# Kernel optimization log

Hardware: AMD Instinct MI355X
Metric: run time of the kernel (lower is better)

## Reference

```python
import jax, jax.numpy as jnp
import numpy as np

P = 256  # patch_size (init kwarg)


def _unfold3s2(g):
    # g: [B,1,P,P] -> [B,9,L], kernel 3, stride 2, torch Unfold ordering (kh outer, kw inner)
    B = g.shape[0]
    n = (P - 3) // 2 + 1
    cols = [g[:, 0, di:di + 2 * n - 1:2, dj:dj + 2 * n - 1:2]
            for di in range(3) for dj in range(3)]  # each [B,n,n]
    return jnp.stack(cols, axis=1).reshape(B, 9, n * n)


def _fold3s2(patches):
    # patches: [..., 9, L] -> [..., P, P], overlap-add (torch Fold, kernel 3, stride 2)
    lead = patches.shape[:-2]
    n = (P - 3) // 2 + 1
    p = patches.reshape(*lead, 3, 3, n, n)
    out = jnp.zeros((*lead, P, P), patches.dtype)
    for di in range(3):
        for dj in range(3):
            out = out.at[..., di:di + 2 * n - 1:2, dj:dj + 2 * n - 1:2].add(p[..., di, dj, :, :])
    return out


def _maxpool3x3(x):
    # MaxPool2d(3, stride=1, padding=1) on NCHW
    return jax.lax.reduce_window(x, -jnp.inf, jax.lax.max,
                                 (1, 1, 3, 3), (1, 1, 1, 1),
                                 [(0, 0), (0, 0), (1, 1), (1, 1)])


def setup_inputs() -> dict:
    key = jax.random.key(0)
    k1, k2 = jax.random.split(key)
    x = jax.random.uniform(k1, (2, 3, P, P), dtype=jnp.float32)
    ref = jax.random.uniform(k2, (2, 3, P, P), dtype=jnp.float32)
    return {"x": x, "ref": ref, "k": 4}


def reference(x, ref, k):
    B = x.shape[0]
    L = ((P - 3) // 2 + 1) ** 2
    # grayscale proxies
    x_gray = jnp.max(_maxpool3x3(x), axis=1, keepdims=True) - jnp.min(x, axis=1, keepdims=True)
    ref_gray = jnp.mean(ref, axis=1, keepdims=True)
    input_patch = _unfold3s2(x_gray)   # [B,9,L]
    ref_patch = _unfold3s2(ref_gray)   # [B,9,L]
    # faithful to original: mean over patch index (dim 2), norm of UNCENTERED patches over dim 1
    input_norm = (input_patch - jnp.mean(input_patch, axis=2, keepdims=True)) \
        / jnp.linalg.norm(input_patch, axis=1, keepdims=True)
    ref_norm = (ref_patch - jnp.mean(ref_patch, axis=2, keepdims=True)) \
        / jnp.linalg.norm(ref_patch, axis=1, keepdims=True)
    ncc = jnp.einsum('bpl,bpm->blm', input_norm, ref_norm)  # [B,L,L]
    _, idx = jax.lax.top_k(ncc, k)                           # idx: [B,L,k]
    # gather best-matching ref patches for all k at once: [B,k,9,L]
    idx_t = jnp.transpose(idx, (0, 2, 1))                    # [B,k,L]
    ind = jnp.broadcast_to(idx_t[:, :, None, :], (B, k, 9, L))
    src = jnp.broadcast_to(ref_patch[:, None], (B, k, 9, L))
    gathered = jnp.take_along_axis(src, ind, axis=3)         # [B,k,9,L]
    folded = _fold3s2(gathered)                              # [B,k,P,P]
    return jnp.concatenate([x, folded], axis=1)              # [B,3+k,P,P]
```

## Files before the change

kernel.cpp:

```cpp
#include <hip/hip_runtime.h>
#include <math.h>
#include <float.h>

#define PSZ 256
#define NPATCH 127
#define L 16129
#define KTOP 4
#define TMAIN 256
#define RPT 2
#define ROWS_PER_BLOCK (TMAIN * RPT)
#define NROWBLK 32
#define NS 32
#define SEGLEN 505
#define MSTRIDE 508
#define ROWPAD 16384
#define GRP 8

typedef float f2 __attribute__((ext_vector_type(2)));

static constexpr size_t OFF_CMAX = 0;
static constexpr size_t OFF_CMIN = OFF_CMAX + 2 * PSZ * PSZ;
static constexpr size_t OFF_REFG = OFF_CMIN + 2 * PSZ * PSZ;
static constexpr size_t OFF_XG   = OFF_REFG + 2 * PSZ * PSZ;
static constexpr size_t OFF_MUI  = OFF_XG   + 2 * PSZ * PSZ;
static constexpr size_t OFF_MUR  = OFF_MUI  + 20;
static constexpr size_t OFF_A    = OFF_MUR  + 20;
static constexpr size_t OFF_B    = OFF_A    + 290324;
static constexpr size_t OFF_BT   = OFF_B    + 290324;
static constexpr size_t OFF_IDX  = OFF_BT   + 290324;
static constexpr size_t OFF_G4   = OFF_IDX  + 2 * L * 4;
static constexpr size_t OFF_PV   = OFF_G4   + 2 * L * 4;
static constexpr size_t OFF_PI   = OFF_PV   + (size_t)2 * NS * ROWPAD * 4;

__device__ __forceinline__ void insg(float rm, int gb,
    float& g0, float& g1, float& g2, float& g3,
    int& i0, int& i1, int& i2, int& i3) {
  bool c0 = rm > g0, c1 = rm > g1, c2 = rm > g2, c3 = rm > g3;
  g3 = c2 ? g2 : (c3 ? rm : g3);  i3 = c2 ? i2 : (c3 ? gb : i3);
  g2 = c1 ? g1 : (c2 ? rm : g2);  i2 = c1 ? i1 : (c2 ? gb : i2);
  g1 = c0 ? g0 : (c1 ? rm : g1);  i1 = c0 ? i0 : (c1 ? gb : i1);
  g0 = c0 ? rm : g0;              i0 = c0 ? gb : i0;
}

__device__ __forceinline__ void ins4c(float v, int m,
    float& v0, float& v1, float& v2, float& v3,
    int& x0, int& x1, int& x2, int& x3) {
  bool c0 = (v > v0) || (v == v0 && m < x0);
  bool c1 = (v > v1) || (v == v1 && m < x1);
  bool c2 = (v > v2) || (v == v2 && m < x2);
  bool c3 = (v > v3) || (v == v3 && m < x3);
  v3 = c2 ? v2 : (c3 ? v : v3);  x3 = c2 ? x2 : (c3 ? m : x3);
  v2 = c1 ? v1 : (c2 ? v : v2);  x2 = c1 ? x1 : (c2 ? m : x2);
  v1 = c0 ? v0 : (c1 ? v : v1);  x1 = c0 ? x0 : (c1 ? m : x1);
  v0 = c0 ? v : v0;              x0 = c0 ? m : x0;
}

__global__ void k1_pixel(const float* __restrict__ x, const float* __restrict__ ref,
                         float* __restrict__ ws, float* __restrict__ out) {
  int id = blockIdx.x * 256 + threadIdx.x;
  if (id >= 2 * PSZ * PSZ) return;
  int b = id >> 16;
  int pix = id & 0xFFFF;
  const float* xb = x + (size_t)b * 3 * PSZ * PSZ + pix;
  float c0 = xb[0], c1 = xb[PSZ * PSZ], c2 = xb[2 * PSZ * PSZ];
  ws[OFF_CMAX + id] = fmaxf(fmaxf(c0, c1), c2);
  ws[OFF_CMIN + id] = fminf(fminf(c0, c1), c2);
  const float* rb = ref + (size_t)b * 3 * PSZ * PSZ + pix;
  ws[OFF_REFG + id] = (rb[0] + rb[PSZ * PSZ] + rb[2 * PSZ * PSZ]) / 3.0f;
  float* ob = out + (size_t)b * 7 * PSZ * PSZ + pix;
  ob[0] = c0; ob[PSZ * PSZ] = c1; ob[2 * PSZ * PSZ] = c2;
}

__global__ void k2_gray(float* __restrict__ ws) {
  int id = blockIdx.x * 256 + threadIdx.x;
  if (id >= 2 * PSZ * PSZ) return;
  int b = id >> 16;
  int pix = id & 0xFFFF;
  int y = pix >> 8, xx = pix & 255;
  const float* cm = ws + OFF_CMAX + ((size_t)b << 16);
  float m = -3.402823466e+38f;
  for (int dy = -1; dy <= 1; ++dy) {
    int yy = y + dy;
    if (yy < 0 || yy > 255) continue;
    for (int dx = -1; dx <= 1; ++dx) {
      int xc = xx + dx;
      if (xc < 0 || xc > 255) continue;
      m = fmaxf(m, cm[yy * PSZ + xc]);
    }
  }
  ws[OFF_XG + id] = m - ws[OFF_CMIN + id];
}

__global__ void k4_mean(float* __restrict__ ws) {
  __shared__ double sm[256];
  int which = blockIdx.x / 18;
  int bp = blockIdx.x % 18;
  int b = bp / 9, p = bp % 9;
  int di = p / 3, dj = p % 3;
  const float* g = ws + (which ? OFF_REFG : OFF_XG) + ((size_t)b << 16);
  double s = 0.0;
  for (int l = threadIdx.x; l < L; l += 256) {
    int i = l / NPATCH, j = l % NPATCH;
    s += (double)g[(2 * i + di) * PSZ + 2 * j + dj];
  }
  sm[threadIdx.x] = s;
  __syncthreads();
  for (int st = 128; st > 0; st >>= 1) {
    if ((int)threadIdx.x < st) sm[threadIdx.x] += sm[threadIdx.x + st];
    __syncthreads();
  }
  if (threadIdx.x == 0)
    ws[(which ? OFF_MUR : OFF_MUI) + bp] = (float)(sm[0] / (double)L);
}

__global__ void k5_norm(float* __restrict__ ws) {
  int id = blockIdx.x * 256 + threadIdx.x;
  if (id >= 2 * L) return;
  int b = id / L, l = id % L;
  int i = l / NPATCH, j = l % NPATCH;
  const float* xg = ws + OFF_XG + ((size_t)b << 16);
  const float* rg = ws + OFF_REFG + ((size_t)b << 16);
  float vi[9], vr[9];
  float si = 0.f, sr = 0.f;
#pragma unroll
  for (int p = 0; p < 9; ++p) {
    int di = p / 3, dj = p % 3;
    vi[p] = xg[(2 * i + di) * PSZ + 2 * j + dj];
    vr[p] = rg[(2 * i + di) * PSZ + 2 * j + dj];
    si += vi[p] * vi[p];
    sr += vr[p] * vr[p];
  }
  float ni = sqrtf(si), nr = sqrtf(sr);
#pragma unroll
  for (int p = 0; p < 9; ++p) {
    float mi = ws[OFF_MUI + b * 9 + p];
    float mr = ws[OFF_MUR + b * 9 + p];
    float bn = (vr[p] - mr) / nr;
    ws[OFF_A + ((size_t)b * L + l) * 9 + p] = (vi[p] - mi) / ni;
    ws[OFF_B + ((size_t)b * 9 + p) * L + l] = bn;
    ws[OFF_BT + ((size_t)b * L + l) * 9 + p] = bn;
  }
}

__global__ __launch_bounds__(TMAIN, 2) void k6_topk(float* __restrict__ ws) {
  __shared__ float lds[9 * MSTRIDE];

  int bid = blockIdx.x;
  int seg = bid % NS;
  int rowblk = (bid / NS) % NROWBLK;
  int b = bid / (NS * NROWBLK);
  int m0 = seg * SEGLEN;
  int mend = m0 + SEGLEN;
  if (mend > L) mend = L;
  int mlen = mend - m0;

  const float* Bg = ws + OFF_B + (size_t)b * 9 * L + m0;
  for (int p = 0; p < 9; ++p)
    for (int mm = threadIdx.x; mm < mlen; mm += TMAIN)
      lds[p * MSTRIDE + mm] = Bg[(size_t)p * L + mm];
  __syncthreads();

  int row0 = rowblk * ROWS_PER_BLOCK + threadIdx.x * RPT;
  int r0 = row0 < L - 1 ? row0 : L - 1;
  int r1 = row0 + 1 < L - 1 ? row0 + 1 : L - 1;
  float a0[9], a1[9];
  {
    const float* Ap0 = ws + OFF_A + ((size_t)b * L + r0) * 9;
    const float* Ap1 = ws + OFF_A + ((size_t)b * L + r1) * 9;
#pragma unroll
    for (int p = 0; p < 9; ++p) { a0[p] = Ap0[p]; a1[p] = Ap1[p]; }
  }

  float g00 = -FLT_MAX, g01 = g00, g02 = g00, g03 = g00;
  float g10 = g00, g11 = g00, g12 = g00, g13 = g00;
  int i00 = 0, i01 = 0, i02 = 0, i03 = 0;
  int i10 = 0, i11 = 0, i12 = 0, i13 = 0;

  int ngrp = mlen >> 3;
  for (int g = 0; g < ngrp; ++g) {
    int mm = g << 3;
    f2 s0a, s0b, s0c, s0d, s1a, s1b, s1c, s1d;
#pragma unroll
    for (int p = 0; p < 9; ++p) {
      const float* base = &lds[p * MSTRIDE + mm];
      f2 b0 = *(const f2*)(base + 0);
      f2 b1 = *(const f2*)(base + 2);
      f2 b2 = *(const f2*)(base + 4);
      f2 b3 = *(const f2*)(base + 6);
      f2 va = {a0[p], a0[p]};
      f2 vb = {a1[p], a1[p]};
      if (p == 0) {
        s0a = va * b0; s0b = va * b1; s0c = va * b2; s0d = va * b3;
        s1a = vb * b0; s1b = vb * b1; s1c = vb * b2; s1d = vb * b3;
      } else {
        s0a = __builtin_elementwise_fma(va, b0, s0a);
        s0b = __builtin_elementwise_fma(va, b1, s0b);
        s0c = __builtin_elementwise_fma(va, b2, s0c);
        s0d = __builtin_elementwise_fma(va, b3, s0d);
        s1a = __builtin_elementwise_fma(vb, b0, s1a);
        s1b = __builtin_elementwise_fma(vb, b1, s1b);
        s1c = __builtin_elementwise_fma(vb, b2, s1c);
        s1d = __builtin_elementwise_fma(vb, b3, s1d);
      }
    }
    f2 rv0 = __builtin_elementwise_max(__builtin_elementwise_max(s0a, s0b),
                                       __builtin_elementwise_max(s0c, s0d));
    f2 rv1 = __builtin_elementwise_max(__builtin_elementwise_max(s1a, s1b),
                                       __builtin_elementwise_max(s1c, s1d));
    float rm0 = fmaxf(rv0.x, rv0.y);
    float rm1 = fmaxf(rv1.x, rv1.y);
    int gb = m0 + mm;
    insg(rm0, gb, g00, g01, g02, g03, i00, i01, i02, i03);
    insg(rm1, gb, g10, g11, g12, g13, i10, i11, i12, i13);
  }
  int tb = ngrp << 3;
  if (tb < mlen) {
    float rt0 = -FLT_MAX, rt1 = -FLT_MAX;
    for (int mm = tb; mm < mlen; ++mm) {
      float bb = lds[mm];
      float sv0 = a0[0] * bb, sv1 = a1[0] * bb;
#pragma unroll
      for (int p = 1; p < 9; ++p) {
        bb = lds[p * MSTRIDE + mm];
        sv0 = fmaf(a0[p], bb, sv0); sv1 = fmaf(a1[p], bb, sv1);
      }
      rt0 = fmaxf(rt0, sv0); rt1 = fmaxf(rt1, sv1);
    }
    insg(rt0, m0 + tb, g00, g01, g02, g03, i00, i01, i02, i03);
    insg(rt1, m0 + tb, g10, g11, g12, g13, i10, i11, i12, i13);
  }

  int* wsi = (int*)ws;
  if (row0 < L) {
    size_t base = (((size_t)b * NS + seg) * ROWPAD + row0) * 4;
    ws[OFF_PV + base + 0] = g00; ws[OFF_PV + base + 1] = g01;
    ws[OFF_PV + base + 2] = g02; ws[OFF_PV + base + 3] = g03;
    wsi[OFF_PI + base + 0] = i00; wsi[OFF_PI + base + 1] = i01;
    wsi[OFF_PI + base + 2] = i02; wsi[OFF_PI + base + 3] = i03;
  }
  if (row0 + 1 < L) {
    size_t base = (((size_t)b * NS + seg) * ROWPAD + row0 + 1) * 4;
    ws[OFF_PV + base + 0] = g10; ws[OFF_PV + base + 1] = g11;
    ws[OFF_PV + base + 2] = g12; ws[OFF_PV + base + 3] = g13;
    wsi[OFF_PI + base + 0] = i10; wsi[OFF_PI + base + 1] = i11;
    wsi[OFF_PI + base + 2] = i12; wsi[OFF_PI + base + 3] = i13;
  }
}

__global__ void k7a_groups(float* __restrict__ ws) {
  int id = blockIdx.x * 256 + threadIdx.x;
  if (id >= 2 * L) return;
  int b = id / L, row = id % L;
  float v0 = -FLT_MAX, v1 = v0, v2 = v0, v3 = v0;
  int x0 = 0x7FFFFFFF, x1 = x0, x2 = x0, x3 = x0;
  const int* wsi_c = (const int*)ws;
  for (int s = 0; s < NS; ++s) {
    size_t base = (((size_t)b * NS + s) * ROWPAD + row) * 4;
#pragma unroll
    for (int q = 0; q < 4; ++q) {
      float val = ws[OFF_PV + base + q];
      int gb = wsi_c[OFF_PI + base + q];
      ins4c(val, gb, v0, v1, v2, v3, x0, x1, x2, x3);
    }
  }
  int* wsi = (int*)ws;
  size_t gb4 = OFF_G4 + (size_t)id * 4;
  wsi[gb4] = x0; wsi[gb4 + 1] = x1; wsi[gb4 + 2] = x2; wsi[gb4 + 3] = x3;
}

__global__ void k7b_recover(float* __restrict__ ws) {
  int id = blockIdx.x * 256 + threadIdx.x;
  if (id >= 2 * L) return;
  int b = id / L, row = id % L;
  float a[9];
  const float* Ap = ws + OFF_A + ((size_t)b * L + row) * 9;
#pragma unroll
  for (int p = 0; p < 9; ++p) a[p] = Ap[p];
  const int* wsi_c = (const int*)ws;
  float v0 = -FLT_MAX, v1 = v0, v2 = v0, v3 = v0;
  int x0 = 0x7FFFFFFF, x1 = x0, x2 = x0, x3 = x0;
#pragma unroll
  for (int slot = 0; slot < 4; ++slot) {
    int gb = wsi_c[OFF_G4 + (size_t)id * 4 + slot];
    int ge = gb + GRP; if (ge > L) ge = L;
    for (int mm = gb; mm < ge; ++mm) {
      const float* bt = ws + OFF_BT + ((size_t)b * L + mm) * 9;
      float s = a[0] * bt[0];
#pragma unroll
      for (int p = 1; p < 9; ++p) s = fmaf(a[p], bt[p], s);
      ins4c(s, mm, v0, v1, v2, v3, x0, x1, x2, x3);
    }
  }
  int* wsi = (int*)ws;
  size_t ib = OFF_IDX + (size_t)id * 4;
  wsi[ib] = x0; wsi[ib + 1] = x1; wsi[ib + 2] = x2; wsi[ib + 3] = x3;
}

__global__ void k8_fold(const float* __restrict__ ws, float* __restrict__ out) {
  int id = blockIdx.x * 256 + threadIdx.x;
  if (id >= 2 * KTOP * PSZ * PSZ) return;
  int b = id / (KTOP * PSZ * PSZ);
  int rem = id % (KTOP * PSZ * PSZ);
  int kk = rem >> 16;
  int pix = rem & 0xFFFF;
  int y = pix >> 8, xx = pix & 255;
  const int* wsi = (const int*)ws;
  const float* rg = ws + OFF_REFG + ((size_t)b << 16);
  float acc = 0.f;
  for (int di = 0; di < 3; ++di) {
    int yy = y - di;
    if (yy < 0 || (yy & 1) || (yy >> 1) >= NPATCH) continue;
    int i = yy >> 1;
    for (int dj = 0; dj < 3; ++dj) {
      int xc = xx - dj;
      if (xc < 0 || (xc & 1) || (xc >> 1) >= NPATCH) continue;
      int j = xc >> 1;
      int l = i * NPATCH + j;
      int m = wsi[OFF_IDX + ((size_t)b * L + l) * 4 + kk];
      int mi = m / NPATCH, mj = m % NPATCH;
      acc += rg[(2 * mi + di) * PSZ + 2 * mj + dj];
    }
  }
  out[(((size_t)b * 7 + 3 + kk) * PSZ + y) * PSZ + xx] = acc;
}

extern "C" void kernel_launch(void* const* d_in, const int* in_sizes, int n_in,
                              void* d_out, int out_size, void* d_ws, size_t ws_size,
                              hipStream_t stream) {
  const float* x = (const float*)d_in[0];
  const float* ref = (const float*)d_in[1];
  float* ws = (float*)d_ws;
  float* out = (float*)d_out;

  k1_pixel<<<512, 256, 0, stream>>>(x, ref, ws, out);
  k2_gray<<<512, 256, 0, stream>>>(ws);
  k4_mean<<<36, 256, 0, stream>>>(ws);
  k5_norm<<<(2 * L + 255) / 256, 256, 0, stream>>>(ws);
  k6_topk<<<2 * NROWBLK * NS, TMAIN, 0, stream>>>(ws);
  k7a_groups<<<(2 * L + 255) / 256, 256, 0, stream>>>(ws);
  k7b_recover<<<(2 * L + 255) / 256, 256, 0, stream>>>(ws);
  k8_fold<<<(2 * KTOP * PSZ * PSZ + 255) / 256, 256, 0, stream>>>(ws, out);
}
```

Baseline: 244.5 us.

## Fuse top-k merge kernels, use packed FMA asm, widen mean reduction

Merges the group-merge and recovery kernels into one, dropping the intermediate group-index buffer and one launch. The top-k inner loop now uses inline v_pk_fma/v_pk_mul asm with float4 LDS loads and pre-splatted A vectors, and replaces the packed max tree with scalar fmaxf. Launch bounds on the top-k kernel are relaxed to one block per SIMD, trading occupancy for registers. The mean kernel uses 1024 threads with contiguous 16-element chunks per thread.

```diff
diff --git a/kernel.cpp b/kernel.cpp
--- a/kernel.cpp
+++ b/kernel.cpp
@@ -18,6 +18,17 @@
 
 typedef float f2 __attribute__((ext_vector_type(2)));
 
+__device__ __forceinline__ f2 pk_fma(f2 a, f2 b, f2 c) {
+  f2 d;
+  asm("v_pk_fma_f32 %0, %1, %2, %3" : "=v"(d) : "v"(a), "v"(b), "v"(c));
+  return d;
+}
+__device__ __forceinline__ f2 pk_mul(f2 a, f2 b) {
+  f2 d;
+  asm("v_pk_mul_f32 %0, %1, %2" : "=v"(d) : "v"(a), "v"(b));
+  return d;
+}
+
 static constexpr size_t OFF_CMAX = 0;
 static constexpr size_t OFF_CMIN = OFF_CMAX + 2 * PSZ * PSZ;
 static constexpr size_t OFF_REFG = OFF_CMIN + 2 * PSZ * PSZ;
@@ -28,8 +39,7 @@
 static constexpr size_t OFF_B    = OFF_A    + 290324;
 static constexpr size_t OFF_BT   = OFF_B    + 290324;
 static constexpr size_t OFF_IDX  = OFF_BT   + 290324;
-static constexpr size_t OFF_G4   = OFF_IDX  + 2 * L * 4;
-static constexpr size_t OFF_PV   = OFF_G4   + 2 * L * 4;
+static constexpr size_t OFF_PV   = OFF_IDX  + 2 * L * 4;
 static constexpr size_t OFF_PI   = OFF_PV   + (size_t)2 * NS * ROWPAD * 4;
 
 __device__ __forceinline__ void insg(float rm, int gb,
@@ -92,24 +102,30 @@
 }
 
 __global__ void k4_mean(float* __restrict__ ws) {
-  __shared__ double sm[256];
+  __shared__ double sm[1024];
   int which = blockIdx.x / 18;
   int bp = blockIdx.x % 18;
   int b = bp / 9, p = bp % 9;
   int di = p / 3, dj = p % 3;
   const float* g = ws + (which ? OFF_REFG : OFF_XG) + ((size_t)b << 16);
+  int t = threadIdx.x;
   double s = 0.0;
-  for (int l = threadIdx.x; l < L; l += 256) {
-    int i = l / NPATCH, j = l % NPATCH;
-    s += (double)g[(2 * i + di) * PSZ + 2 * j + dj];
-  }
-  sm[threadIdx.x] = s;
+  int l0 = t * 16;
+  if (l0 < L) {
+    int l1 = l0 + 16 < L ? l0 + 16 : L;
+    int i = l0 / NPATCH, j = l0 % NPATCH;
+    for (int l = l0; l < l1; ++l) {
+      s += (double)g[(2 * i + di) * PSZ + 2 * j + dj];
+      if (++j == NPATCH) { j = 0; ++i; }
+    }
+  }
+  sm[t] = s;
   __syncthreads();
-  for (int st = 128; st > 0; st >>= 1) {
-    if ((int)threadIdx.x < st) sm[threadIdx.x] += sm[threadIdx.x + st];
+  for (int st = 512; st > 0; st >>= 1) {
+    if (t < st) sm[t] += sm[t + st];
     __syncthreads();
   }
-  if (threadIdx.x == 0)
+  if (t == 0)
     ws[(which ? OFF_MUR : OFF_MUI) + bp] = (float)(sm[0] / (double)L);
 }
 
@@ -142,7 +158,7 @@
   }
 }
 
-__global__ __launch_bounds__(TMAIN, 2) void k6_topk(float* __restrict__ ws) {
+__global__ __launch_bounds__(TMAIN, 1) void k6_topk(float* __restrict__ ws) {
   __shared__ float lds[9 * MSTRIDE];
 
   int bid = blockIdx.x;
@@ -163,12 +179,16 @@
   int row0 = rowblk * ROWS_PER_BLOCK + threadIdx.x * RPT;
   int r0 = row0 < L - 1 ? row0 : L - 1;
   int r1 = row0 + 1 < L - 1 ? row0 + 1 : L - 1;
-  float a0[9], a1[9];
+  f2 va[9], vb[9];
   {
     const float* Ap0 = ws + OFF_A + ((size_t)b * L + r0) * 9;
     const float* Ap1 = ws + OFF_A + ((size_t)b * L + r1) * 9;
 #pragma unroll
-    for (int p = 0; p < 9; ++p) { a0[p] = Ap0[p]; a1[p] = Ap1[p]; }
+    for (int p = 0; p < 9; ++p) {
+      float a0 = Ap0[p], a1 = Ap1[p];
+      va[p].x = a0; va[p].y = a0;
+      vb[p].x = a1; vb[p].y = a1;
+    }
   }
 
   float g00 = -FLT_MAX, g01 = g00, g02 = g00, g03 = g00;
@@ -182,33 +202,26 @@
     f2 s0a, s0b, s0c, s0d, s1a, s1b, s1c, s1d;
 #pragma unroll
     for (int p = 0; p < 9; ++p) {
-      const float* base = &lds[p * MSTRIDE + mm];
-      f2 b0 = *(const f2*)(base + 0);
-      f2 b1 = *(const f2*)(base + 2);
-      f2 b2 = *(const f2*)(base + 4);
-      f2 b3 = *(const f2*)(base + 6);
-      f2 va = {a0[p], a0[p]};
-      f2 vb = {a1[p], a1[p]};
+      const float4* bp4 = reinterpret_cast<const float4*>(&lds[p * MSTRIDE + mm]);
+      float4 q0 = bp4[0], q1 = bp4[1];
+      f2 b0 = {q0.x, q0.y}, b1 = {q0.z, q0.w};
+      f2 b2 = {q1.x, q1.y}, b3 = {q1.z, q1.w};
       if (p == 0) {
-        s0a = va * b0; s0b = va * b1; s0c = va * b2; s0d = va * b3;
-        s1a = vb * b0; s1b = vb * b1; s1c = vb * b2; s1d = vb * b3;
+        s0a = pk_mul(va[0], b0); s0b = pk_mul(va[0], b1);
+        s0c = pk_mul(va[0], b2); s0d = pk_mul(va[0], b3);
+        s1a = pk_mul(vb[0], b0); s1b = pk_mul(vb[0], b1);
+        s1c = pk_mul(vb[0], b2); s1d = pk_mul(vb[0], b3);
       } else {
-        s0a = __builtin_elementwise_fma(va, b0, s0a);
-        s0b = __builtin_elementwise_fma(va, b1, s0b);
-        s0c = __builtin_elementwise_fma(va, b2, s0c);
-        s0d = __builtin_elementwise_fma(va, b3, s0d);
-        s1a = __builtin_elementwise_fma(vb, b0, s1a);
-        s1b = __builtin_elementwise_fma(vb, b1, s1b);
-        s1c = __builtin_elementwise_fma(vb, b2, s1c);
-        s1d = __builtin_elementwise_fma(vb, b3, s1d);
+        s0a = pk_fma(va[p], b0, s0a); s0b = pk_fma(va[p], b1, s0b);
+        s0c = pk_fma(va[p], b2, s0c); s0d = pk_fma(va[p], b3, s0d);
+        s1a = pk_fma(vb[p], b0, s1a); s1b = pk_fma(vb[p], b1, s1b);
+        s1c = pk_fma(vb[p], b2, s1c); s1d = pk_fma(vb[p], b3, s1d);
       }
     }
-    f2 rv0 = __builtin_elementwise_max(__builtin_elementwise_max(s0a, s0b),
-                                       __builtin_elementwise_max(s0c, s0d));
-    f2 rv1 = __builtin_elementwise_max(__builtin_elementwise_max(s1a, s1b),
-                                       __builtin_elementwise_max(s1c, s1d));
-    float rm0 = fmaxf(rv0.x, rv0.y);
-    float rm1 = fmaxf(rv1.x, rv1.y);
+    float rm0 = fmaxf(fmaxf(fmaxf(s0a.x, s0a.y), fmaxf(s0b.x, s0b.y)),
+                      fmaxf(fmaxf(s0c.x, s0c.y), fmaxf(s0d.x, s0d.y)));
+    float rm1 = fmaxf(fmaxf(fmaxf(s1a.x, s1a.y), fmaxf(s1b.x, s1b.y)),
+                      fmaxf(fmaxf(s1c.x, s1c.y), fmaxf(s1d.x, s1d.y)));
     int gb = m0 + mm;
     insg(rm0, gb, g00, g01, g02, g03, i00, i01, i02, i03);
     insg(rm1, gb, g10, g11, g12, g13, i10, i11, i12, i13);
@@ -218,11 +231,11 @@
     float rt0 = -FLT_MAX, rt1 = -FLT_MAX;
     for (int mm = tb; mm < mlen; ++mm) {
       float bb = lds[mm];
-      float sv0 = a0[0] * bb, sv1 = a1[0] * bb;
+      float sv0 = va[0].x * bb, sv1 = vb[0].x * bb;
 #pragma unroll
       for (int p = 1; p < 9; ++p) {
         bb = lds[p * MSTRIDE + mm];
-        sv0 = fmaf(a0[p], bb, sv0); sv1 = fmaf(a1[p], bb, sv1);
+        sv0 = fmaf(va[p].x, bb, sv0); sv1 = fmaf(vb[p].x, bb, sv1);
       }
       rt0 = fmaxf(rt0, sv0); rt1 = fmaxf(rt1, sv1);
     }
@@ -247,13 +260,14 @@
   }
 }
 
-__global__ void k7a_groups(float* __restrict__ ws) {
+__global__ void k7_merge(float* __restrict__ ws) {
   int id = blockIdx.x * 256 + threadIdx.x;
   if (id >= 2 * L) return;
   int b = id / L, row = id % L;
+  const int* wsi_c = (const int*)ws;
+
   float v0 = -FLT_MAX, v1 = v0, v2 = v0, v3 = v0;
   int x0 = 0x7FFFFFFF, x1 = x0, x2 = x0, x3 = x0;
-  const int* wsi_c = (const int*)ws;
   for (int s = 0; s < NS; ++s) {
     size_t base = (((size_t)b * NS + s) * ROWPAD + row) * 4;
 #pragma unroll
@@ -263,37 +277,30 @@
       ins4c(val, gb, v0, v1, v2, v3, x0, x1, x2, x3);
     }
   }
-  int* wsi = (int*)ws;
-  size_t gb4 = OFF_G4 + (size_t)id * 4;
-  wsi[gb4] = x0; wsi[gb4 + 1] = x1; wsi[gb4 + 2] = x2; wsi[gb4 + 3] = x3;
-}
-
-__global__ void k7b_recover(float* __restrict__ ws) {
-  int id = blockIdx.x * 256 + threadIdx.x;
-  if (id >= 2 * L) return;
-  int b = id / L, row = id % L;
+
   float a[9];
   const float* Ap = ws + OFF_A + ((size_t)b * L + row) * 9;
 #pragma unroll
   for (int p = 0; p < 9; ++p) a[p] = Ap[p];
-  const int* wsi_c = (const int*)ws;
-  float v0 = -FLT_MAX, v1 = v0, v2 = v0, v3 = v0;
-  int x0 = 0x7FFFFFFF, x1 = x0, x2 = x0, x3 = x0;
+
+  int gbs[4] = {x0, x1, x2, x3};
+  float w0 = -FLT_MAX, w1 = w0, w2 = w0, w3 = w0;
+  int y0 = 0x7FFFFFFF, y1 = y0, y2 = y0, y3 = y0;
 #pragma unroll
   for (int slot = 0; slot < 4; ++slot) {
-    int gb = wsi_c[OFF_G4 + (size_t)id * 4 + slot];
+    int gb = gbs[slot];
     int ge = gb + GRP; if (ge > L) ge = L;
     for (int mm = gb; mm < ge; ++mm) {
       const float* bt = ws + OFF_BT + ((size_t)b * L + mm) * 9;
       float s = a[0] * bt[0];
 #pragma unroll
       for (int p = 1; p < 9; ++p) s = fmaf(a[p], bt[p], s);
-      ins4c(s, mm, v0, v1, v2, v3, x0, x1, x2, x3);
+      ins4c(s, mm, w0, w1, w2, w3, y0, y1, y2, y3);
     }
   }
   int* wsi = (int*)ws;
   size_t ib = OFF_IDX + (size_t)id * 4;
-  wsi[ib] = x0; wsi[ib + 1] = x1; wsi[ib + 2] = x2; wsi[ib + 3] = x3;
+  wsi[ib] = y0; wsi[ib + 1] = y1; wsi[ib + 2] = y2; wsi[ib + 3] = y3;
 }
 
 __global__ void k8_fold(const float* __restrict__ ws, float* __restrict__ out) {
@@ -334,10 +341,9 @@
 
   k1_pixel<<<512, 256, 0, stream>>>(x, ref, ws, out);
   k2_gray<<<512, 256, 0, stream>>>(ws);
-  k4_mean<<<36, 256, 0, stream>>>(ws);
+  k4_mean<<<36, 1024, 0, stream>>>(ws);
   k5_norm<<<(2 * L + 255) / 256, 256, 0, stream>>>(ws);
   k6_topk<<<2 * NROWBLK * NS, TMAIN, 0, stream>>>(ws);
-  k7a_groups<<<(2 * L + 255) / 256, 256, 0, stream>>>(ws);
-  k7b_recover<<<(2 * L + 255) / 256, 256, 0, stream>>>(ws);
+  k7_merge<<<(2 * L + 255) / 256, 256, 0, stream>>>(ws);
   k8_fold<<<(2 * KTOP * PSZ * PSZ + 255) / 256, 256, 0, stream>>>(ws, out);
 }
```

Result: faster. 238.4 us (-2.5%).
